# Kernel optimization log

Measured on AMD Instinct MI355X. Metric: run time of the kernel, lower is better.

The kernel has to match this reference:

```python
import jax, jax.numpy as jnp
from jax import lax
import numpy as np

B, T, N, HORIZON = 64, 12, 512, 12
IN_DIM = 1; OUT_DIM = 1; YCOV = 1
RNN = 64; MEM_NUM = 20; MEM_DIM = 64; EMB = 10; CHEB_K = 3
DEC_DIM = RNN + MEM_DIM  # 128


def _xavier(key, shape):
    fan_in, fan_out = shape[0], shape[-1]
    std = float(np.sqrt(2.0 / (fan_in + fan_out)))
    return jax.random.normal(key, shape, dtype=jnp.float32) * std


def _cheb_feats(A, x, batched):
    mm = (lambda a, v: jnp.einsum('bnm,bmc->bnc', a, v)) if batched else (lambda a, v: jnp.einsum('nm,bmc->bnc', a, v))
    gs = [x, mm(A, x)]
    for _ in range(CHEB_K - 2):
        gs.append(2.0 * mm(A, gs[-1]) - gs[-2])
    return jnp.concatenate(gs, axis=-1)


def _agcn(x, A, W, b, batched):
    return _cheb_feats(A, x, batched) @ W + b


def _cell(x, state, A, Wg, bg, Wu, bu, batched):
    # AGCRN GRU cell
    hid = state.shape[-1]
    inp = jnp.concatenate([x, state], axis=-1)
    z_r = jax.nn.sigmoid(_agcn(inp, A, Wg, bg, batched))
    z, r = z_r[..., :hid], z_r[..., hid:]
    cand = jnp.concatenate([x, z * state], axis=-1)
    hc = jnp.tanh(_agcn(cand, A, Wu, bu, batched))
    return r * state + (1.0 - r) * hc


def _encode(x, A, Wg, bg, Wu, bu):
    # x: [B,T,N,C] -> last hidden state [B,N,RNN]
    xt = jnp.swapaxes(x, 0, 1)  # [T,B,N,C]
    init = jnp.zeros((x.shape[0], x.shape[2], RNN), x.dtype)
    def step(state, xt_):
        h = _cell(xt_, state, A, Wg, bg, Wu, bu, batched=False)
        return h, None
    h_t, _ = lax.scan(step, init, xt)
    return h_t


def _query_memory(h_t, Memory, Wq):
    q = h_t @ Wq                                   # [B,N,mem_dim]
    att = jax.nn.softmax(q @ Memory.T, axis=-1)    # [B,N,mem_num]
    value = att @ Memory                           # [B,N,mem_dim]
    _, ind = lax.top_k(att, 2)
    pos = Memory[ind[..., 0]]                      # [B,N,mem_dim]
    return value, pos


def setup_inputs() -> dict:
    key = jax.random.key(0)
    ks = jax.random.split(key, 20)
    x = jax.random.normal(ks[0], (B, T, N, IN_DIM), dtype=jnp.float32)
    x_cov = jax.random.normal(ks[1], (B, T, N, 1), dtype=jnp.float32)
    x_his = jax.random.normal(ks[2], (B, T, N, IN_DIM), dtype=jnp.float32)
    y_cov = jax.random.normal(ks[3], (B, HORIZON, N, YCOV), dtype=jnp.float32)
    a = jax.random.uniform(ks[4], (N, N), dtype=jnp.float32)
    adj = a / jnp.sum(a, axis=-1, keepdims=True)
    enc_in = IN_DIM + RNN
    dec_in = OUT_DIM + YCOV + DEC_DIM
    return {
        'x': x, 'x_cov': x_cov, 'x_his': x_his, 'y_cov': y_cov, 'adj': adj,
        'enc_gate_W': _xavier(ks[5], (CHEB_K * enc_in, 2 * RNN)),
        'enc_gate_b': jnp.zeros((2 * RNN,), jnp.float32),
        'enc_upd_W': _xavier(ks[6], (CHEB_K * enc_in, RNN)),
        'enc_upd_b': jnp.zeros((RNN,), jnp.float32),
        'dec_gate_W': _xavier(ks[7], (CHEB_K * dec_in, 2 * DEC_DIM)),
        'dec_gate_b': jnp.zeros((2 * DEC_DIM,), jnp.float32),
        'dec_upd_W': _xavier(ks[8], (CHEB_K * dec_in, DEC_DIM)),
        'dec_upd_b': jnp.zeros((DEC_DIM,), jnp.float32),
        'Memory': _xavier(ks[9], (MEM_NUM, MEM_DIM)),
        'Wq': _xavier(ks[10], (RNN, MEM_DIM)),
        'hyper_W': _xavier(ks[11], (DEC_DIM, EMB)),
        'hyper_b': jnp.zeros((EMB,), jnp.float32),
        'lat_W': _xavier(ks[12], (MEM_DIM, 1)),
        'lat_b': jnp.zeros((1,), jnp.float32),
        'proj_W': _xavier(ks[13], (DEC_DIM, OUT_DIM)),
        'proj_b': jnp.zeros((OUT_DIM,), jnp.float32),
    }


def reference(x, x_cov, x_his, y_cov, adj,
              enc_gate_W, enc_gate_b, enc_upd_W, enc_upd_b,
              dec_gate_W, dec_gate_b, dec_upd_W, dec_upd_b,
              Memory, Wq, hyper_W, hyper_b, lat_W, lat_b, proj_W, proj_b):
    # --- encoder on x and x_his (shared weights, single static support) ---
    h_t = _encode(x, adj, enc_gate_W, enc_gate_b, enc_upd_W, enc_upd_b)
    h_att, pos = _query_memory(h_t, Memory, Wq)
    h_his_t = _encode(x_his, adj, enc_gate_W, enc_gate_b, enc_upd_W, enc_upd_b)
    _, pos_his = _query_memory(h_his_t, Memory, Wq)
    # schema==1 latent distance head (sigmoid activation)
    latent_dis = jax.nn.sigmoid(((pos - pos_his) @ lat_W + lat_b)[..., 0])  # [B,N]
    # --- adaptive decoder support from hypernetwork ---
    h_aug = jnp.concatenate([h_t, h_att], axis=-1)          # [B,N,DEC_DIM]
    node_emb = h_aug @ hyper_W + hyper_b                    # [B,N,EMB]
    support = jax.nn.softmax(jax.nn.relu(jnp.einsum('bnc,bmc->bnm', node_emb, node_emb)), axis=-1)  # [B,N,N]
    # --- decoder rollout (inference path, no teacher forcing) ---
    go0 = jnp.zeros((x.shape[0], N, OUT_DIM), x.dtype)
    ycov_t = jnp.swapaxes(y_cov, 0, 1)  # [HORIZON,B,N,YCOV]
    def dec_step(carry, yc):
        go, h = carry
        xt = jnp.concatenate([go, yc], axis=-1)
        h = _cell(xt, h, support, dec_gate_W, dec_gate_b, dec_upd_W, dec_upd_b, batched=True)
        go = h @ proj_W + proj_b
        return (go, h), go
    _, outs = lax.scan(dec_step, (go0, h_aug), ycov_t)
    output = jnp.swapaxes(outs, 0, 1)  # [B,HORIZON,N,OUT_DIM]
    return output, latent_dis
```

## Files before the change

### kernel.cpp

```cpp
#include <hip/hip_runtime.h>
#include <hip/hip_bf16.h>


typedef __attribute__((ext_vector_type(8))) short s8v;
typedef __attribute__((ext_vector_type(4))) float f4v;
typedef __attribute__((ext_vector_type(4))) unsigned short u4v;

__device__ __forceinline__ float b2f(unsigned short u){
  union{unsigned int i; float f;} v; v.i = ((unsigned int)u)<<16; return v.f;
}
__device__ __forceinline__ unsigned short f2b(float f){
  union{float f; unsigned int i;} v; v.f = f;
  unsigned int r = v.i + 0x7fff + ((v.i >> 16) & 1);
  return (unsigned short)(r >> 16);
}

__global__ void k_zero16(uint4* p, int n){
  int i = blockIdx.x*256 + threadIdx.x;
  if (i < n) p[i] = make_uint4(0,0,0,0);
}


__global__ void k_reorderF(const float* __restrict__ W, float* __restrict__ Wr,
                           int HC, int NEX, int SEGW, int J){
  int idx = blockIdx.x*256 + threadIdx.x;
  int K = 3*SEGW;
  if (idx >= K*J) return;
  int k = idx / J, j = idx - k*J;
  int seg = k / SEGW, c = k - seg*SEGW;
  int CIN = HC + NEX;
  float v = 0.f;
  if (c < HC)       v = W[(size_t)(seg*CIN + NEX + c)*J + j];
  else if (c < CIN) v = W[(size_t)(seg*CIN + (c-HC))*J + j];
  Wr[(size_t)k*J + j] = v;
}

__global__ __launch_bounds__(256) void k_a2e(const float* __restrict__ A,
                                             float* __restrict__ A2e){
  __shared__ __align__(16) float As[32][132];
  __shared__ __align__(16) float Bs[32][132];
  int t = threadIdx.x;
  int r0 = (blockIdx.x & 3) * 128;
  int c0 = (blockIdx.x >> 2) * 128;
  int tr = t & 15, tc = t >> 4;
  float acc[8][8];
  #pragma unroll
  for (int i=0;i<8;i++)
    #pragma unroll
    for (int j=0;j<8;j++) acc[i][j]=0.f;
  for (int k0=0;k0<512;k0+=32){
    #pragma unroll
    for (int i=0;i<4;i++){
      int s = t + i*256;
      int k = s & 31, rq = s >> 5;
      const float* ap = A + (size_t)(r0 + rq*4)*512 + k0 + k;
      float4 v;
      v.x = ap[0]; v.y = ap[512]; v.z = ap[1024]; v.w = ap[1536];
      *(float4*)&As[k][rq*4] = v;
    }
    #pragma unroll
    for (int i=0;i<4;i++){
      int s = t + i*256;
      int k = s >> 5, cq = s & 31;
      float4 v = *(const float4*)(A + (size_t)(k0+k)*512 + c0 + cq*4);
      *(float4*)&Bs[k][cq*4] = v;
    }
    __syncthreads();
    #pragma unroll 8
    for (int k=0;k<32;k++){
      float a[8], b[8];
      *(float4*)&a[0] = *(const float4*)&As[k][tr*4];
      *(float4*)&a[4] = *(const float4*)&As[k][64+tr*4];
      *(float4*)&b[0] = *(const float4*)&Bs[k][tc*4];
      *(float4*)&b[4] = *(const float4*)&Bs[k][64+tc*4];
      #pragma unroll
      for (int i=0;i<8;i++)
        #pragma unroll
        for (int j=0;j<8;j++) acc[i][j] += a[i]*b[j];
    }
    __syncthreads();
  }
  #pragma unroll
  for (int i=0;i<8;i++){
    int r = r0 + (i<4 ? tr*4+i : 64+tr*4+i-4);
    #pragma unroll
    for (int j=0;j<8;j++){
      int c = c0 + (j<4 ? tc*4+j : 64+tc*4+j-4);
      A2e[(size_t)r*512 + c] = 2.f*acc[i][j] - (r==c ? 1.f : 0.f);
    }
  }
}

template<int MODE>
__global__ __launch_bounds__(256) void k_enc(
    const float* __restrict__ A, const float* __restrict__ A2e,
    const float* __restrict__ hsrc,
    const float* __restrict__ xa, const float* __restrict__ xb,
    int tstep, const float* __restrict__ Wr, const float* __restrict__ bias,
    float* __restrict__ zh, float* __restrict__ rbuf, float* __restrict__ henc)
{
  constexpr int J  = (MODE==0) ? 128 : 64;
  constexpr int TN = (MODE==0) ? 8 : 4;
  __shared__ __align__(16) float R1[8704];
  __shared__ __align__(16) float F0t[2][65][66];
  float (*sA)[68]   = (float(*)[68])(R1);
  float (*sA2)[68]  = (float(*)[68])(R1 + 2176);
  float (*sB0)[68]  = (float(*)[68])(R1 + 4352);
  float (*sB1)[68]  = (float(*)[68])(R1 + 6528);
  float (*G12s)[66] = (float(*)[66])(R1);
  const int t = threadIdx.x;
  const int z = blockIdx.x;
  const int rowblk = blockIdx.z;
  const int n0 = rowblk * 64;
  const int tr = t & 15, tc = t >> 4;
  const int xrow = t & 63, xmat = (t >> 6) & 1, xbb = t >> 7;
  const float* xp0 = xa + ((size_t)z*12 + tstep)*512;
  const float* xp1 = xb + ((size_t)z*12 + tstep)*512;

  float acc[2][2][4][4];
  #pragma unroll
  for (int m=0;m<2;m++)
    #pragma unroll
    for (int b=0;b<2;b++)
      #pragma unroll
      for (int i=0;i<4;i++)
        #pragma unroll
        for (int j=0;j<4;j++) acc[m][b][i][j]=0.f;
  float xacc = 0.f;

  for (int k0=0;k0<512;k0+=32){
    #pragma unroll
    for (int i=0;i<2;i++){
      int s = t + i*256;
      int k = s & 31, rq = s >> 5;
      const float* ap  = A   + (size_t)(n0 + rq*4)*512 + k0 + k;
      const float* a2p = A2e + (size_t)(n0 + rq*4)*512 + k0 + k;
      float4 v, w;
      v.x = ap[0];  v.y = ap[512];  v.z = ap[1024];  v.w = ap[1536];
      w.x = a2p[0]; w.y = a2p[512]; w.z = a2p[1024]; w.w = a2p[1536];
      *(float4*)&sA[k][rq*4]  = v;
      *(float4*)&sA2[k][rq*4] = w;
    }
    #pragma unroll
    for (int i=0;i<2;i++){
      int s = t + i*256;
      int k = s >> 4, cq = s & 15;
      *(float4*)&sB0[k][cq*4] = *(const float4*)(hsrc + (size_t)(z*512 + k0 + k)*64 + cq*4);
      *(float4*)&sB1[k][cq*4] = *(const float4*)(hsrc + (size_t)((z+64)*512 + k0 + k)*64 + cq*4);
    }
    if (t < 32)      sB0[t][64]    = xp0[k0 + t];
    else if (t < 64) sB1[t-32][64] = xp1[k0 + t - 32];
    __syncthreads();
    #pragma unroll 4
    for (int k=0;k<32;k++){
      float a1[4], a2[4], b0[4], b1[4];
      *(float4*)&a1[0] = *(const float4*)&sA[k][tr*4];
      *(float4*)&a2[0] = *(const float4*)&sA2[k][tr*4];
      *(float4*)&b0[0] = *(const float4*)&sB0[k][tc*4];
      *(float4*)&b1[0] = *(const float4*)&sB1[k][tc*4];
      #pragma unroll
      for (int i=0;i<4;i++)
        #pragma unroll
        for (int j=0;j<4;j++){
          acc[0][0][i][j] += a1[i]*b0[j];
          acc[0][1][i][j] += a1[i]*b1[j];
          acc[1][0][i][j] += a2[i]*b0[j];
          acc[1][1][i][j] += a2[i]*b1[j];
        }
      float am = xmat ? sA2[k][xrow] : sA[k][xrow];
      xacc += am * (xbb ? sB1[k][64] : sB0[k][64]);
    }
    if ((k0 >> 6) == rowblk){
      const int off = k0 & 63;
      for (int s=t; s<4160; s+=256){
        int sb = (s >= 2080) ? 1 : 0;
        int ss = s - sb*2080;
        int c = ss >> 5, kk = ss & 31;
        F0t[sb][c][off + kk] = sb ? sB1[kk][c] : sB0[kk][c];
      }
    }
    __syncthreads();
  }

  for (int bbi=0; bbi<2; bbi++){
    #pragma unroll
    for (int m=0;m<2;m++)
      #pragma unroll
      for (int j=0;j<4;j++){
        float4 v;
        v.x = acc[m][bbi][0][j]; v.y = acc[m][bbi][1][j];
        v.z = acc[m][bbi][2][j]; v.w = acc[m][bbi][3][j];
        *(float4*)&G12s[m*65 + tc*4 + j][tr*4] = v;
      }
    if (xbb == bbi) G12s[xmat*65 + 64][xrow] = xacc;
    __syncthreads();

    float acc2[4][TN];
    #pragma unroll
    for (int i=0;i<4;i++)
      #pragma unroll
      for (int jj=0;jj<TN;jj++) acc2[i][jj]=0.f;
    const int j0 = tc*TN;

    #pragma unroll 4
    for (int c=0;c<65;c++){
      float a[4], w[TN];
      *(float4*)&a[0] = *(const float4*)&F0t[bbi][c][tr*4];
      #pragma unroll
      for (int q=0;q<TN;q+=4) *(float4*)&w[q] = *(const float4*)(Wr + (size_t)c*J + j0 + q);
      #pragma unroll
      for (int i=0;i<4;i++)
        #pragma unroll
        for (int jj=0;jj<TN;jj++) acc2[i][jj] += a[i]*w[jj];
    }
    #pragma unroll 4
    for (int c=0;c<65;c++){
      float a[4], w[TN];
      *(float4*)&a[0] = *(const float4*)&G12s[c][tr*4];
      #pragma unroll
      for (int q=0;q<TN;q+=4) *(float4*)&w[q] = *(const float4*)(Wr + (size_t)(68+c)*J + j0 + q);
      #pragma unroll
      for (int i=0;i<4;i++)
        #pragma unroll
        for (int jj=0;jj<TN;jj++) acc2[i][jj] += a[i]*w[jj];
    }
    #pragma unroll 4
    for (int c=0;c<65;c++){
      float a[4], w[TN];
      *(float4*)&a[0] = *(const float4*)&G12s[65+c][tr*4];
      #pragma unroll
      for (int q=0;q<TN;q+=4) *(float4*)&w[q] = *(const float4*)(Wr + (size_t)(136+c)*J + j0 + q);
      #pragma unroll
      for (int i=0;i<4;i++)
        #pragma unroll
        for (int jj=0;jj<TN;jj++) acc2[i][jj] += a[i]*w[jj];
    }

    float bj[TN];
    #pragma unroll
    for (int jj=0;jj<TN;jj++) bj[jj] = bias[j0+jj];
    const int gbase = (z + bbi*64)*512 + n0;
    #pragma unroll
    for (int i=0;i<4;i++){
      const int lr = tr*4 + i;
      const int row = gbase + lr;
      if (MODE == 0){
        float s[8];
        #pragma unroll
        for (int jj=0;jj<TN;jj++) s[jj] = 1.f/(1.f + __expf(-(acc2[i][jj] + bj[jj])));
        if (j0 < 64){
          float4 o0, o1;
          o0.x = s[0]*F0t[bbi][j0+0][lr]; o0.y = s[1]*F0t[bbi][j0+1][lr];
          o0.z = s[2]*F0t[bbi][j0+2][lr]; o0.w = s[3]*F0t[bbi][j0+3][lr];
          o1.x = s[4]*F0t[bbi][j0+4][lr]; o1.y = s[5]*F0t[bbi][j0+5][lr];
          o1.z = s[6]*F0t[bbi][j0+6][lr]; o1.w = s[7]*F0t[bbi][j0+7][lr];
          *(float4*)(zh + (size_t)row*64 + j0)     = o0;
          *(float4*)(zh + (size_t)row*64 + j0 + 4) = o1;
        } else {
          float4 o0, o1;
          o0.x=s[0]; o0.y=s[1]; o0.z=s[2]; o0.w=s[3];
          o1.x=s[4]; o1.y=s[5]; o1.z=s[6]; o1.w=s[7];
          *(float4*)(rbuf + (size_t)row*64 + j0 - 64) = o0;
          *(float4*)(rbuf + (size_t)row*64 + j0 - 60) = o1;
        }
      } else {
        float4 h4 = *(const float4*)(henc + (size_t)row*64 + j0);
        float4 r4 = *(const float4*)(rbuf + (size_t)row*64 + j0);
        float hv[4] = {h4.x,h4.y,h4.z,h4.w};
        float rv[4] = {r4.x,r4.y,r4.z,r4.w};
        float ov[4];
        #pragma unroll
        for (int jj=0;jj<4;jj++){
          float hc = 1.f - 2.f/(__expf(2.f*(acc2[i][jj] + bj[jj])) + 1.f);
          ov[jj] = rv[jj]*hv[jj] + (1.f - rv[jj])*hc;
        }
        float4 o; o.x=ov[0]; o.y=ov[1]; o.z=ov[2]; o.w=ov[3];
        *(float4*)(henc + (size_t)row*64 + j0) = o;
      }
    }
    __syncthreads();
  }
}


__global__ void k_reorderB(const float* __restrict__ W, unsigned short* __restrict__ Wr,
                           int HC, int NEX, int C, int KP, int J){
  int idx = blockIdx.x*256 + threadIdx.x;
  if (idx >= J*KP) return;
  int j = idx / KP, kp = idx - j*KP;
  float v = 0.f;
  if (kp < 3*C){
    int seg = kp / C, c = kp - seg*C;
    int CIN = HC + NEX;
    if (c < HC)       v = W[(size_t)(seg*CIN + NEX + c)*J + j];
    else if (c < CIN) v = W[(size_t)(seg*CIN + (c-HC))*J + j];
  }
  Wr[(size_t)j*KP + kp] = f2b(v);
}

template<int C16, bool BETA>
__global__ __launch_bounds__(256) void k_mmB(
    const unsigned short* __restrict__ M, long long mstride,
    unsigned short* fC, int C3, int xseg, int oseg,
    unsigned short* fR, int KP, float alpha)
{
  constexpr int C = C16*16;
  constexpr int BIT = (C*4 + 255)/256;
  __shared__ unsigned short Bs[C*40];
  const int t = threadIdx.x;
  const int w = t >> 6, L = t & 63, lm = L & 15, q = L >> 4;
  const int bb = blockIdx.z;
  const int n0 = blockIdx.x * 128;
  const unsigned short* Mb = M + (size_t)bb * mstride;
  unsigned short* fCb = fC + (size_t)bb * C3 * 512;
  const unsigned short* Xb = fCb + (size_t)xseg * C * 512;
  const unsigned short* Yb = fCb;
  unsigned short* Ob = fCb + (size_t)oseg * C * 512;
  const int rw = n0 + w*32;

  f4v acc[2][C16];
  #pragma unroll
  for (int i=0;i<2;i++)
    #pragma unroll
    for (int j=0;j<C16;j++)
      #pragma unroll
      for (int r=0;r<4;r++) acc[i][j][r] = 0.f;

  s8v breg[BIT];
  const size_t ar0 = (size_t)(rw + lm)*512 + q*8;
  const size_t ar1 = (size_t)(rw + 16 + lm)*512 + q*8;

  #pragma unroll
  for (int i=0;i<BIT;i++){
    int s = t + i*256;
    if (s < C*4) breg[i] = *(const s8v*)(Xb + (size_t)(s>>2)*512 + (s&3)*8);
  }
  s8v a0 = *(const s8v*)(Mb + ar0);
  s8v a1 = *(const s8v*)(Mb + ar1);

  for (int ks=0; ks<16; ks++){
    #pragma unroll
    for (int i=0;i<BIT;i++){
      int s = t + i*256;
      if (s < C*4) *(s8v*)&Bs[(s>>2)*40 + (s&3)*8] = breg[i];
    }
    __syncthreads();
    const int kn = (ks < 15) ? (ks+1)*32 : 0;
    #pragma unroll
    for (int i=0;i<BIT;i++){
      int s = t + i*256;
      if (s < C*4) breg[i] = *(const s8v*)(Xb + (size_t)(s>>2)*512 + kn + (s&3)*8);
    }
    s8v a0n = *(const s8v*)(Mb + ar0 + kn);
    s8v a1n = *(const s8v*)(Mb + ar1 + kn);
    #pragma unroll
    for (int ct=0; ct<C16; ct++){
      s8v b = *(const s8v*)&Bs[(ct*16+lm)*40 + q*8];
      acc[0][ct] = __builtin_amdgcn_mfma_f32_16x16x32_bf16(a0, b, acc[0][ct], 0,0,0);
      acc[1][ct] = __builtin_amdgcn_mfma_f32_16x16x32_bf16(a1, b, acc[1][ct], 0,0,0);
    }
    __syncthreads();
    a0 = a0n; a1 = a1n;
  }
  #pragma unroll
  for (int rt=0; rt<2; rt++){
    const int m0 = rw + rt*16 + q*4;
    #pragma unroll
    for (int ct=0; ct<C16; ct++){
      const int c = ct*16 + lm;
      u4v o;
      if (BETA){
        u4v y = *(const u4v*)(Yb + (size_t)c*512 + m0);
        #pragma unroll
        for (int r=0;r<4;r++) o[r] = f2b(alpha*acc[rt][ct][r] - b2f(y[r]));
      } else {
        #pragma unroll
        for (int r=0;r<4;r++) o[r] = f2b(acc[rt][ct][r]);
      }
      *(u4v*)(Ob + (size_t)c*512 + m0) = o;
      const size_t rbase = (size_t)(bb*512 + m0)*KP + oseg*C + c;
      #pragma unroll
      for (int r=0;r<4;r++) fR[rbase + (size_t)r*KP] = o[r];
    }
  }
}

template<int KSTEPS, int JT16, int MODE, int HC>
__global__ __launch_bounds__(256) void k_gwB(
    unsigned short* fR, int KP,
    const unsigned short* __restrict__ Wr, const float* __restrict__ bias,
    unsigned short* fC, int C3,
    float* hC, float* rbuf)
{
  constexpr int JT = JT16*16;
  constexpr int BIT = JT*4/256;
  __shared__ unsigned short Bs[JT*40];
  const int t = threadIdx.x;
  const int w = t >> 6, L = t & 63, lm = L & 15, q = L >> 4;
  const int row0 = blockIdx.x * 128;
  const int j0 = blockIdx.y * JT;
  const int rw = row0 + w*32;

  f4v acc[2][JT16];
  #pragma unroll
  for (int i=0;i<2;i++)
    #pragma unroll
    for (int j=0;j<JT16;j++)
      #pragma unroll
      for (int r=0;r<4;r++) acc[i][j][r] = 0.f;

  s8v breg[BIT];
  const unsigned short* Wb = Wr + (size_t)j0*KP;
  const size_t ar0 = (size_t)(rw + lm)*KP + q*8;
  const size_t ar1 = (size_t)(rw + 16 + lm)*KP + q*8;

  #pragma unroll
  for (int i=0;i<BIT;i++){
    int s = t + i*256;
    breg[i] = *(const s8v*)(Wb + (size_t)(s>>2)*KP + (s&3)*8);
  }
  s8v a0 = *(const s8v*)(fR + ar0);
  s8v a1 = *(const s8v*)(fR + ar1);

  for (int ks=0; ks<KSTEPS; ks++){
    #pragma unroll
    for (int i=0;i<BIT;i++){
      int s = t + i*256;
      *(s8v*)&Bs[(s>>2)*40 + (s&3)*8] = breg[i];
    }
    __syncthreads();
    const int kn = (ks < KSTEPS-1) ? (ks+1)*32 : 0;
    #pragma unroll
    for (int i=0;i<BIT;i++){
      int s = t + i*256;
      breg[i] = *(const s8v*)(Wb + (size_t)(s>>2)*KP + kn + (s&3)*8);
    }
    s8v a0n = *(const s8v*)(fR + ar0 + kn);
    s8v a1n = *(const s8v*)(fR + ar1 + kn);
    #pragma unroll
    for (int ct=0; ct<JT16; ct++){
      s8v b = *(const s8v*)&Bs[(ct*16+lm)*40 + q*8];
      acc[0][ct] = __builtin_amdgcn_mfma_f32_16x16x32_bf16(a0, b, acc[0][ct], 0,0,0);
      acc[1][ct] = __builtin_amdgcn_mfma_f32_16x16x32_bf16(a1, b, acc[1][ct], 0,0,0);
    }
    __syncthreads();
    a0 = a0n; a1 = a1n;
  }
  #pragma unroll
  for (int rt=0; rt<2; rt++){
    const int m0 = rw + rt*16 + q*4;
    const int bb = m0 >> 9, n = m0 & 511;
    #pragma unroll
    for (int ct=0; ct<JT16; ct++){
      const int j = j0 + ct*16 + lm;
      const float bj = bias[j];
      if (MODE == 0){
        if (j < HC){
          f4v h4 = *(const f4v*)(hC + ((size_t)bb*HC + j)*512 + n);
          u4v o;
          #pragma unroll
          for (int r=0;r<4;r++){
            float s = 1.f/(1.f + __expf(-(acc[rt][ct][r] + bj)));
            float zh = s * h4[r];
            o[r] = f2b(zh);
            fR[(size_t)(m0+r)*KP + j] = o[r];
          }
          *(u4v*)(fC + ((size_t)bb*C3 + j)*512 + n) = o;
        } else {
          f4v rv;
          #pragma unroll
          for (int r=0;r<4;r++) rv[r] = 1.f/(1.f + __expf(-(acc[rt][ct][r] + bj)));
          *(f4v*)(rbuf + ((size_t)bb*HC + (j-HC))*512 + n) = rv;
        }
      } else {
        f4v h4 = *(const f4v*)(hC + ((size_t)bb*HC + j)*512 + n);
        f4v r4 = *(const f4v*)(rbuf + ((size_t)bb*HC + j)*512 + n);
        u4v o; f4v hn;
        #pragma unroll
        for (int r=0;r<4;r++){
          float e = __expf(2.f*(acc[rt][ct][r] + bj));
          float hc_ = 1.f - 2.f/(e + 1.f);
          hn[r] = r4[r]*h4[r] + (1.f - r4[r])*hc_;
          o[r] = f2b(hn[r]);
          fR[(size_t)(m0+r)*KP + j] = o[r];
        }
        *(f4v*)(hC + ((size_t)bb*HC + j)*512 + n) = hn;
        *(u4v*)(fC + ((size_t)bb*C3 + j)*512 + n) = o;
      }
    }
  }
}


__global__ void k_extras_dec(const float* __restrict__ yc,
    unsigned short* fR, unsigned short* fC, int tstep){
  int rr = blockIdx.x*256 + threadIdx.x;
  int bb = rr >> 9, n = rr & 511;
  unsigned short u = f2b(yc[((size_t)bb*12 + tstep)*512 + n]);
  fR[(size_t)rr*448 + 129] = u;
  fC[((size_t)bb*432 + 129)*512 + n] = u;
}
__global__ void k_fix_go(unsigned short* fR, unsigned short* fC){
  int rr = blockIdx.x*256 + threadIdx.x;
  int bb = rr >> 9, n = rr & 511;
  fR[(size_t)rr*448 + 128] = 0;
  fC[((size_t)bb*432 + 128)*512 + n] = 0;
}

__global__ __launch_bounds__(256) void k_query(const float* __restrict__ hR,
      const float* __restrict__ Wq, const float* __restrict__ Mem,
      float* __restrict__ hCd, unsigned short* fR, unsigned short* fC,
      int* __restrict__ it, int* __restrict__ ih){
  int sub = threadIdx.x >> 6, lane = threadIdx.x & 63;
  int row = blockIdx.x*4 + sub;
  __shared__ float sh[4][64], sq[4][64], ss[4][20];
  float hv = hR[(size_t)row*64 + lane];
  sh[sub][lane] = hv;
  __syncthreads();
  float qv = 0.f;
  for (int c=0;c<64;c++) qv += sh[sub][c]*Wq[c*64 + lane];
  sq[sub][lane] = qv;
  __syncthreads();
  if (lane < 20){
    float s = 0.f;
    for (int j=0;j<64;j++) s += sq[sub][j]*Mem[lane*64 + j];
    ss[sub][lane] = s;
  }
  __syncthreads();
  float mx = -1e30f; int am = 0;
  for (int m=0;m<20;m++){ float s = ss[sub][m]; if (s > mx){ mx = s; am = m; } }
  float sum = 0.f;
  for (int m=0;m<20;m++) sum += __expf(ss[sub][m]-mx);
  float inv = 1.f/sum;
  float v = 0.f;
  for (int m=0;m<20;m++) v += __expf(ss[sub][m]-mx)*inv*Mem[m*64 + lane];
  int bb = row >> 9, n = row & 511;
  if (bb < 64){
    hCd[((size_t)bb*128 + lane)*512 + n] = hv;
    hCd[((size_t)bb*128 + 64 + lane)*512 + n] = v;
    fR[(size_t)row*448 + lane] = f2b(hv);
    fR[(size_t)row*448 + 64 + lane] = f2b(v);
    fC[((size_t)bb*432 + lane)*512 + n] = f2b(hv);
    fC[((size_t)bb*432 + 64 + lane)*512 + n] = f2b(v);
    if (lane==0) it[row] = am;
  } else {
    if (lane==0) ih[row - 32768] = am;
  }
}

__global__ void k_latent(const int* __restrict__ it, const int* __restrict__ ih,
                         const float* __restrict__ Mem,
                         const float* __restrict__ lW, const float* __restrict__ lb,
                         float* __restrict__ outl){
  int row = blockIdx.x*256 + threadIdx.x;
  int i1 = it[row], i2 = ih[row];
  float a = lb[0];
  for (int c=0;c<64;c++) a += (Mem[i1*64+c]-Mem[i2*64+c])*lW[c];
  outl[row] = 1.f/(1.f + __expf(-a));
}

__global__ __launch_bounds__(256) void k_emb(const float* __restrict__ hCd,
    const float* __restrict__ hW, const float* __restrict__ hb, float* __restrict__ emb){
  __shared__ float sW[1280];
  int t = threadIdx.x;
  for (int s=t; s<1280; s+=256) sW[s] = hW[s];
  __syncthreads();
  int rr = blockIdx.x*256 + t;
  int bb = rr >> 9, n = rr & 511;
  float a[10];
  #pragma unroll
  for (int e=0;e<10;e++) a[e] = hb[e];
  for (int c=0;c<128;c++){
    float v = hCd[((size_t)bb*128 + c)*512 + n];
    #pragma unroll
    for (int e=0;e<10;e++) a[e] += v*sW[c*10+e];
  }
  #pragma unroll
  for (int e=0;e<10;e++) emb[(size_t)rr*10 + e] = a[e];
}

__global__ __launch_bounds__(256) void k_support(const float* __restrict__ emb,
                                                 unsigned short* __restrict__ sup){
  int b = blockIdx.x >> 9;
  int n = blockIdx.x & 511;
  int t = threadIdx.x;
  __shared__ float se[5120];
  __shared__ float red[8];
  for (int s = t; s < 5120; s += 256) se[s] = emb[(size_t)b*5120 + s];
  __syncthreads();
  float en[10];
  #pragma unroll
  for (int i=0;i<10;i++) en[i] = se[n*10+i];
  float s0=0.f, s1=0.f;
  #pragma unroll
  for (int i=0;i<10;i++){ s0 += en[i]*se[t*10+i]; s1 += en[i]*se[(t+256)*10+i]; }
  s0 = fmaxf(s0, 0.f); s1 = fmaxf(s1, 0.f);
  float mx = fmaxf(s0, s1);
  for (int o=32;o>0;o>>=1) mx = fmaxf(mx, __shfl_down(mx, o));
  if ((t&63)==0) red[t>>6] = mx;
  __syncthreads();
  mx = fmaxf(fmaxf(red[0],red[1]), fmaxf(red[2],red[3]));
  float e0 = __expf(s0-mx), e1 = __expf(s1-mx);
  float sm = e0 + e1;
  for (int o=32;o>0;o>>=1) sm += __shfl_down(sm, o);
  if ((t&63)==0) red[4+(t>>6)] = sm;
  __syncthreads();
  sm = red[4]+red[5]+red[6]+red[7];
  float inv = 1.f/sm;
  size_t base = ((size_t)b*512 + n)*512;
  sup[base + t]       = f2b(e0*inv);
  sup[base + t + 256] = f2b(e1*inv);
}

__global__ __launch_bounds__(256) void k_proj(const float* __restrict__ hCd,
    const float* __restrict__ pW, const float* __restrict__ pb,
    unsigned short* fR, unsigned short* fC, float* __restrict__ out, int tstep){
  __shared__ float sW[128];
  int t = threadIdx.x;
  if (t < 128) sW[t] = pW[t];
  __syncthreads();
  int rr = blockIdx.x*256 + t;
  int bb = rr >> 9, n = rr & 511;
  float a = pb[0];
  for (int c=0;c<128;c++) a += hCd[((size_t)bb*128 + c)*512 + n]*sW[c];
  out[((size_t)bb*12 + tstep)*512 + n] = a;
  unsigned short u = f2b(a);
  fR[(size_t)rr*448 + 128] = u;
  fC[((size_t)bb*432 + 128)*512 + n] = u;
}

extern "C" void kernel_launch(void* const* d_in, const int* in_sizes, int n_in,
                              void* d_out, int out_size, void* d_ws, size_t ws_size,
                              hipStream_t stream) {
  const float* x     = (const float*)d_in[0];
  const float* x_his = (const float*)d_in[2];
  const float* y_cov = (const float*)d_in[3];
  const float* adj   = (const float*)d_in[4];
  const float* egW   = (const float*)d_in[5];
  const float* egb   = (const float*)d_in[6];
  const float* euW   = (const float*)d_in[7];
  const float* eub   = (const float*)d_in[8];
  const float* dgW   = (const float*)d_in[9];
  const float* dgb   = (const float*)d_in[10];
  const float* duW   = (const float*)d_in[11];
  const float* dub   = (const float*)d_in[12];
  const float* Mem   = (const float*)d_in[13];
  const float* Wq    = (const float*)d_in[14];
  const float* hW    = (const float*)d_in[15];
  const float* hb    = (const float*)d_in[16];
  const float* lW    = (const float*)d_in[17];
  const float* lb    = (const float*)d_in[18];
  const float* pW    = (const float*)d_in[19];
  const float* pb    = (const float*)d_in[20];
  float* out  = (float*)d_out;
  float* outl = out + 393216;

  char* base = (char*)d_ws;
  size_t off = 0;
  auto alloc = [&](size_t bytes)->char*{
    char* p = base + off; off = (off + bytes + 255) & ~(size_t)255; return p;
  };
  float* scratch = (float*)alloc(53477376);
  unsigned short* sup = (unsigned short*)scratch;
  float* emb = scratch + 8650752;
  int*   it  = (int*)(scratch + 9961472);
  int*   ih  = it + 32768;
  float* henc = (float*)alloc(16777216);
  float* zhF  = (float*)alloc(16777216);
  float* hCd  = zhF;
  float* rbF  = (float*)alloc(16777216);
  unsigned short* fR = (unsigned short*)alloc(29360128);
  unsigned short* fC = (unsigned short*)alloc(28311552);
  float* a2e = (float*)alloc(1048576);
  float* wr_egF = (float*)alloc(104448);
  float* wr_euF = (float*)alloc(52224);
  unsigned short* wr_dg = (unsigned short*)alloc(229376);
  unsigned short* wr_du = (unsigned short*)alloc(114688);
  if (ws_size < off) return;

  k_zero16<<<4096,256,0,stream>>>((uint4*)henc, 1048576);
  k_zero16<<<7168,256,0,stream>>>((uint4*)fR, 1835008);
  k_zero16<<<6912,256,0,stream>>>((uint4*)fC, 1769472);
  k_a2e<<<16,256,0,stream>>>(adj, a2e);
  k_reorderF<<<102,256,0,stream>>>(egW, wr_egF, 64,1,68,128);
  k_reorderF<<< 51,256,0,stream>>>(euW, wr_euF, 64,1,68,64);
  k_reorderB<<<448,256,0,stream>>>(dgW, wr_dg, 128,2,144,448,256);
  k_reorderB<<<224,256,0,stream>>>(duW, wr_du, 128,2,144,448,128);

  for (int t = 0; t < 12; t++){
    k_enc<0><<<dim3(64,1,8),256,0,stream>>>(adj, a2e, henc, x, x_his, t,
                                            wr_egF, egb, zhF, rbF, nullptr);
    k_enc<1><<<dim3(64,1,8),256,0,stream>>>(adj, a2e, zhF, x, x_his, t,
                                            wr_euF, eub, nullptr, rbF, henc);
  }

  k_query<<<16384,256,0,stream>>>(henc, Wq, Mem, hCd, fR, fC, it, ih);
  k_latent<<<128,256,0,stream>>>(it, ih, Mem, lW, lb, outl);
  k_emb<<<128,256,0,stream>>>(hCd, hW, hb, emb);
  k_support<<<32768,256,0,stream>>>(emb, sup);
  k_fix_go<<<128,256,0,stream>>>(fR, fC);

  for (int t = 0; t < 12; t++){
    k_extras_dec<<<128,256,0,stream>>>(y_cov, fR, fC, t);
    k_mmB<9,false><<<dim3(4,1,64),256,0,stream>>>(sup, 262144, fC, 432, 0, 1, fR, 448, 1.f);
    k_mmB<9,true ><<<dim3(4,1,64),256,0,stream>>>(sup, 262144, fC, 432, 1, 2, fR, 448, 2.f);
    k_gwB<14,16,0,128><<<dim3(256,1),256,0,stream>>>(fR, 448, wr_dg, dgb, fC, 432, hCd, rbF);
    k_mmB<9,false><<<dim3(4,1,64),256,0,stream>>>(sup, 262144, fC, 432, 0, 1, fR, 448, 1.f);
    k_mmB<9,true ><<<dim3(4,1,64),256,0,stream>>>(sup, 262144, fC, 432, 1, 2, fR, 448, 2.f);
    k_gwB<14,8,1,128><<<dim3(256,1),256,0,stream>>>(fR, 448, wr_du, dub, fC, 432, hCd, rbF);
    k_proj<<<128,256,0,stream>>>(hCd, pW, pb, fR, fC, out, t);
  }
}
```

Baseline: 6.503 ms.

## Precompute second Chebyshev support and fuse decoder graph matmuls into one kernel

Adds a one-time batched MFMA kernel that builds the second Chebyshev support 2S²−I in bf16, so each decoder cell computes S·X and S2·X independently in a single fused kernel instead of two dependent launches. This removes the serial dependency and one launch per cell, and halves the per-block row tile to raise parallelism. The encoder kernel also halves its k-tile and reuses one shared buffer for the two Chebyshev feature halves, which cuts LDS use but adds a barrier and doubles loop iterations. The trade-off is extra bf16 rounding in the precomputed S2 and an additional 32MB workspace buffer.

```diff
diff --git a/kernel.cpp b/kernel.cpp
--- a/kernel.cpp
+++ b/kernel.cpp
@@ -101,13 +101,13 @@
 {
   constexpr int J  = (MODE==0) ? 128 : 64;
   constexpr int TN = (MODE==0) ? 8 : 4;
-  __shared__ __align__(16) float R1[8704];
+  __shared__ __align__(16) float R1[4352];
   __shared__ __align__(16) float F0t[2][65][66];
   float (*sA)[68]   = (float(*)[68])(R1);
-  float (*sA2)[68]  = (float(*)[68])(R1 + 2176);
-  float (*sB0)[68]  = (float(*)[68])(R1 + 4352);
-  float (*sB1)[68]  = (float(*)[68])(R1 + 6528);
-  float (*G12s)[66] = (float(*)[66])(R1);
+  float (*sA2)[68]  = (float(*)[68])(R1 + 1088);
+  float (*sB0)[68]  = (float(*)[68])(R1 + 2176);
+  float (*sB1)[68]  = (float(*)[68])(R1 + 3264);
+  float (*G12h)[66] = (float(*)[66])(R1);
   const int t = threadIdx.x;
   const int z = blockIdx.x;
   const int rowblk = blockIdx.z;
@@ -128,11 +128,9 @@
         for (int j=0;j<4;j++) acc[m][b][i][j]=0.f;
   float xacc = 0.f;
 
-  for (int k0=0;k0<512;k0+=32){
-    #pragma unroll
-    for (int i=0;i<2;i++){
-      int s = t + i*256;
-      int k = s & 31, rq = s >> 5;
+  for (int k0=0;k0<512;k0+=16){
+    {
+      int k = t & 15, rq = t >> 4;
       const float* ap  = A   + (size_t)(n0 + rq*4)*512 + k0 + k;
       const float* a2p = A2e + (size_t)(n0 + rq*4)*512 + k0 + k;
       float4 v, w;
@@ -141,18 +139,16 @@
       *(float4*)&sA[k][rq*4]  = v;
       *(float4*)&sA2[k][rq*4] = w;
     }
-    #pragma unroll
-    for (int i=0;i<2;i++){
-      int s = t + i*256;
-      int k = s >> 4, cq = s & 15;
+    {
+      int k = t >> 4, cq = t & 15;
       *(float4*)&sB0[k][cq*4] = *(const float4*)(hsrc + (size_t)(z*512 + k0 + k)*64 + cq*4);
       *(float4*)&sB1[k][cq*4] = *(const float4*)(hsrc + (size_t)((z+64)*512 + k0 + k)*64 + cq*4);
     }
-    if (t < 32)      sB0[t][64]    = xp0[k0 + t];
-    else if (t < 64) sB1[t-32][64] = xp1[k0 + t - 32];
+    if (t < 16)      sB0[t][64]    = xp0[k0 + t];
+    else if (t < 32) sB1[t-16][64] = xp1[k0 + t - 16];
     __syncthreads();
     #pragma unroll 4
-    for (int k=0;k<32;k++){
+    for (int k=0;k<16;k++){
       float a1[4], a2[4], b0[4], b1[4];
       *(float4*)&a1[0] = *(const float4*)&sA[k][tr*4];
       *(float4*)&a2[0] = *(const float4*)&sA2[k][tr*4];
@@ -172,10 +168,10 @@
     }
     if ((k0 >> 6) == rowblk){
       const int off = k0 & 63;
-      for (int s=t; s<4160; s+=256){
-        int sb = (s >= 2080) ? 1 : 0;
-        int ss = s - sb*2080;
-        int c = ss >> 5, kk = ss & 31;
+      for (int s=t; s<2080; s+=256){
+        int sb = (s >= 1040) ? 1 : 0;
+        int ss = s - sb*1040;
+        int c = ss >> 4, kk = ss & 15;
         F0t[sb][c][off + kk] = sb ? sB1[kk][c] : sB0[kk][c];
       }
     }
@@ -184,15 +180,13 @@
 
   for (int bbi=0; bbi<2; bbi++){
     #pragma unroll
-    for (int m=0;m<2;m++)
-      #pragma unroll
-      for (int j=0;j<4;j++){
-        float4 v;
-        v.x = acc[m][bbi][0][j]; v.y = acc[m][bbi][1][j];
-        v.z = acc[m][bbi][2][j]; v.w = acc[m][bbi][3][j];
-        *(float4*)&G12s[m*65 + tc*4 + j][tr*4] = v;
-      }
-    if (xbb == bbi) G12s[xmat*65 + 64][xrow] = xacc;
+    for (int j=0;j<4;j++){
+      float4 v;
+      v.x = acc[0][bbi][0][j]; v.y = acc[0][bbi][1][j];
+      v.z = acc[0][bbi][2][j]; v.w = acc[0][bbi][3][j];
+      *(float4*)&G12h[tc*4 + j][tr*4] = v;
+    }
+    if (xbb == bbi && xmat == 0) G12h[64][xrow] = xacc;
     __syncthreads();
 
     float acc2[4][TN];
@@ -216,7 +210,7 @@
     #pragma unroll 4
     for (int c=0;c<65;c++){
       float a[4], w[TN];
-      *(float4*)&a[0] = *(const float4*)&G12s[c][tr*4];
+      *(float4*)&a[0] = *(const float4*)&G12h[c][tr*4];
       #pragma unroll
       for (int q=0;q<TN;q+=4) *(float4*)&w[q] = *(const float4*)(Wr + (size_t)(68+c)*J + j0 + q);
       #pragma unroll
@@ -224,10 +218,20 @@
         #pragma unroll
         for (int jj=0;jj<TN;jj++) acc2[i][jj] += a[i]*w[jj];
     }
+    __syncthreads();
+    #pragma unroll
+    for (int j=0;j<4;j++){
+      float4 v;
+      v.x = acc[1][bbi][0][j]; v.y = acc[1][bbi][1][j];
+      v.z = acc[1][bbi][2][j]; v.w = acc[1][bbi][3][j];
+      *(float4*)&G12h[tc*4 + j][tr*4] = v;
+    }
+    if (xbb == bbi && xmat == 1) G12h[64][xrow] = xacc;
+    __syncthreads();
     #pragma unroll 4
     for (int c=0;c<65;c++){
       float a[4], w[TN];
-      *(float4*)&a[0] = *(const float4*)&G12s[65+c][tr*4];
+      *(float4*)&a[0] = *(const float4*)&G12h[c][tr*4];
       #pragma unroll
       for (int q=0;q<TN;q+=4) *(float4*)&w[q] = *(const float4*)(Wr + (size_t)(136+c)*J + j0 + q);
       #pragma unroll
@@ -298,89 +302,132 @@
   Wr[(size_t)j*KP + kp] = f2b(v);
 }
 
-template<int C16, bool BETA>
-__global__ __launch_bounds__(256) void k_mmB(
-    const unsigned short* __restrict__ M, long long mstride,
-    unsigned short* fC, int C3, int xseg, int oseg,
-    unsigned short* fR, int KP, float alpha)
+__global__ __launch_bounds__(256) void k_sup2(const unsigned short* __restrict__ S,
+                                              unsigned short* __restrict__ S2){
+  __shared__ unsigned short Bs[128*40];
+  const int t = threadIdx.x;
+  const int w = t >> 6, L = t & 63, lm = L & 15, q = L >> 4;
+  const int bb = blockIdx.z;
+  const int n0 = blockIdx.x * 128;
+  const int m0 = blockIdx.y * 128;
+  const unsigned short* Sb = S + (size_t)bb * 262144;
+  unsigned short* S2b = S2 + (size_t)bb * 262144;
+  f4v acc[2][8];
+  #pragma unroll
+  for (int i=0;i<2;i++)
+    #pragma unroll
+    for (int j=0;j<8;j++)
+      #pragma unroll
+      for (int r=0;r<4;r++) acc[i][j][r] = 0.f;
+  for (int k0=0;k0<512;k0+=32){
+    #pragma unroll
+    for (int i=0;i<2;i++){
+      int s = t + i*256;
+      int kk = s >> 4, mg = s & 15;
+      s8v v = *(const s8v*)(Sb + (size_t)(k0+kk)*512 + m0 + mg*8);
+      #pragma unroll
+      for (int e=0;e<8;e++) Bs[(mg*8+e)*40 + kk] = ((unsigned short*)&v)[e];
+    }
+    __syncthreads();
+    s8v a0 = *(const s8v*)(Sb + (size_t)(n0 + w*32 + lm)*512 + k0 + q*8);
+    s8v a1 = *(const s8v*)(Sb + (size_t)(n0 + w*32 + 16 + lm)*512 + k0 + q*8);
+    #pragma unroll
+    for (int ct=0;ct<8;ct++){
+      s8v b = *(const s8v*)&Bs[(ct*16+lm)*40 + q*8];
+      acc[0][ct] = __builtin_amdgcn_mfma_f32_16x16x32_bf16(a0, b, acc[0][ct], 0,0,0);
+      acc[1][ct] = __builtin_amdgcn_mfma_f32_16x16x32_bf16(a1, b, acc[1][ct], 0,0,0);
+    }
+    __syncthreads();
+  }
+  #pragma unroll
+  for (int rt=0;rt<2;rt++){
+    const int row = n0 + w*32 + rt*16 + q*4;
+    #pragma unroll
+    for (int ct=0;ct<8;ct++){
+      const int col = m0 + ct*16 + lm;
+      #pragma unroll
+      for (int r=0;r<4;r++){
+        float v = 2.f*acc[rt][ct][r] - ((row+r)==col ? 1.f : 0.f);
+        S2b[(size_t)(row+r)*512 + col] = f2b(v);
+      }
+    }
+  }
+}
+
+__global__ __launch_bounds__(256) void k_mmB2(
+    const unsigned short* __restrict__ M1, const unsigned short* __restrict__ M2,
+    unsigned short* fC, unsigned short* fR)
 {
-  constexpr int C = C16*16;
-  constexpr int BIT = (C*4 + 255)/256;
+  constexpr int C = 144;
   __shared__ unsigned short Bs[C*40];
   const int t = threadIdx.x;
   const int w = t >> 6, L = t & 63, lm = L & 15, q = L >> 4;
   const int bb = blockIdx.z;
-  const int n0 = blockIdx.x * 128;
-  const unsigned short* Mb = M + (size_t)bb * mstride;
-  unsigned short* fCb = fC + (size_t)bb * C3 * 512;
-  const unsigned short* Xb = fCb + (size_t)xseg * C * 512;
-  const unsigned short* Yb = fCb;
-  unsigned short* Ob = fCb + (size_t)oseg * C * 512;
-  const int rw = n0 + w*32;
-
-  f4v acc[2][C16];
+  const int n0 = blockIdx.x * 64;
+  const unsigned short* M1b = M1 + (size_t)bb * 262144;
+  const unsigned short* M2b = M2 + (size_t)bb * 262144;
+  unsigned short* fCb = fC + (size_t)bb * 432 * 512;
+  const unsigned short* Xb = fCb;
+  unsigned short* O1 = fCb + (size_t)C * 512;
+  unsigned short* O2 = fCb + (size_t)2 * C * 512;
+  const int rw = n0 + w*16;
+
+  f4v acc[2][9];
   #pragma unroll
   for (int i=0;i<2;i++)
     #pragma unroll
-    for (int j=0;j<C16;j++)
+    for (int j=0;j<9;j++)
       #pragma unroll
       for (int r=0;r<4;r++) acc[i][j][r] = 0.f;
 
-  s8v breg[BIT];
-  const size_t ar0 = (size_t)(rw + lm)*512 + q*8;
-  const size_t ar1 = (size_t)(rw + 16 + lm)*512 + q*8;
-
-  #pragma unroll
-  for (int i=0;i<BIT;i++){
+  s8v breg[3];
+  const size_t ar = (size_t)(rw + lm)*512 + q*8;
+  #pragma unroll
+  for (int i=0;i<3;i++){
     int s = t + i*256;
     if (s < C*4) breg[i] = *(const s8v*)(Xb + (size_t)(s>>2)*512 + (s&3)*8);
   }
-  s8v a0 = *(const s8v*)(Mb + ar0);
-  s8v a1 = *(const s8v*)(Mb + ar1);
+  s8v a1 = *(const s8v*)(M1b + ar);
+  s8v a2 = *(const s8v*)(M2b + ar);
 
   for (int ks=0; ks<16; ks++){
     #pragma unroll
-    for (int i=0;i<BIT;i++){
+    for (int i=0;i<3;i++){
       int s = t + i*256;
       if (s < C*4) *(s8v*)&Bs[(s>>2)*40 + (s&3)*8] = breg[i];
     }
     __syncthreads();
     const int kn = (ks < 15) ? (ks+1)*32 : 0;
     #pragma unroll
-    for (int i=0;i<BIT;i++){
+    for (int i=0;i<3;i++){
       int s = t + i*256;
       if (s < C*4) breg[i] = *(const s8v*)(Xb + (size_t)(s>>2)*512 + kn + (s&3)*8);
     }
-    s8v a0n = *(const s8v*)(Mb + ar0 + kn);
-    s8v a1n = *(const s8v*)(Mb + ar1 + kn);
-    #pragma unroll
-    for (int ct=0; ct<C16; ct++){
+    s8v a1n = *(const s8v*)(M1b + ar + kn);
+    s8v a2n = *(const s8v*)(M2b + ar + kn);
+    #pragma unroll
+    for (int ct=0; ct<9; ct++){
       s8v b = *(const s8v*)&Bs[(ct*16+lm)*40 + q*8];
-      acc[0][ct] = __builtin_amdgcn_mfma_f32_16x16x32_bf16(a0, b, acc[0][ct], 0,0,0);
-      acc[1][ct] = __builtin_amdgcn_mfma_f32_16x16x32_bf16(a1, b, acc[1][ct], 0,0,0);
-    }
-    __syncthreads();
-    a0 = a0n; a1 = a1n;
-  }
-  #pragma unroll
-  for (int rt=0; rt<2; rt++){
-    const int m0 = rw + rt*16 + q*4;
-    #pragma unroll
-    for (int ct=0; ct<C16; ct++){
-      const int c = ct*16 + lm;
-      u4v o;
-      if (BETA){
-        u4v y = *(const u4v*)(Yb + (size_t)c*512 + m0);
-        #pragma unroll
-        for (int r=0;r<4;r++) o[r] = f2b(alpha*acc[rt][ct][r] - b2f(y[r]));
-      } else {
-        #pragma unroll
-        for (int r=0;r<4;r++) o[r] = f2b(acc[rt][ct][r]);
-      }
-      *(u4v*)(Ob + (size_t)c*512 + m0) = o;
-      const size_t rbase = (size_t)(bb*512 + m0)*KP + oseg*C + c;
-      #pragma unroll
-      for (int r=0;r<4;r++) fR[rbase + (size_t)r*KP] = o[r];
+      acc[0][ct] = __builtin_amdgcn_mfma_f32_16x16x32_bf16(a1, b, acc[0][ct], 0,0,0);
+      acc[1][ct] = __builtin_amdgcn_mfma_f32_16x16x32_bf16(a2, b, acc[1][ct], 0,0,0);
+    }
+    __syncthreads();
+    a1 = a1n; a2 = a2n;
+  }
+  const int m0 = rw + q*4;
+  #pragma unroll
+  for (int ct=0; ct<9; ct++){
+    const int c = ct*16 + lm;
+    u4v o1, o2;
+    #pragma unroll
+    for (int r=0;r<4;r++){ o1[r] = f2b(acc[0][ct][r]); o2[r] = f2b(acc[1][ct][r]); }
+    *(u4v*)(O1 + (size_t)c*512 + m0) = o1;
+    *(u4v*)(O2 + (size_t)c*512 + m0) = o2;
+    const size_t rb = (size_t)(bb*512 + m0)*448;
+    #pragma unroll
+    for (int r=0;r<4;r++){
+      fR[rb + (size_t)r*448 + 144 + c] = o1[r];
+      fR[rb + (size_t)r*448 + 288 + c] = o2[r];
     }
   }
 }
@@ -660,11 +707,11 @@
   auto alloc = [&](size_t bytes)->char*{
     char* p = base + off; off = (off + bytes + 255) & ~(size_t)255; return p;
   };
-  float* scratch = (float*)alloc(53477376);
-  unsigned short* sup = (unsigned short*)scratch;
-  float* emb = scratch + 8650752;
-  int*   it  = (int*)(scratch + 9961472);
-  int*   ih  = it + 32768;
+  unsigned short* sup  = (unsigned short*)alloc(33554432);
+  unsigned short* sup2 = (unsigned short*)alloc(33554432);
+  float* emb  = (float*)alloc(1310720);
+  int*   it   = (int*)alloc(131072);
+  int*   ih   = (int*)alloc(131072);
   float* henc = (float*)alloc(16777216);
   float* zhF  = (float*)alloc(16777216);
   float* hCd  = zhF;
@@ -698,15 +745,14 @@
   k_latent<<<128,256,0,stream>>>(it, ih, Mem, lW, lb, outl);
   k_emb<<<128,256,0,stream>>>(hCd, hW, hb, emb);
   k_support<<<32768,256,0,stream>>>(emb, sup);
+  k_sup2<<<dim3(4,4,64),256,0,stream>>>(sup, sup2);
   k_fix_go<<<128,256,0,stream>>>(fR, fC);
 
   for (int t = 0; t < 12; t++){
     k_extras_dec<<<128,256,0,stream>>>(y_cov, fR, fC, t);
-    k_mmB<9,false><<<dim3(4,1,64),256,0,stream>>>(sup, 262144, fC, 432, 0, 1, fR, 448, 1.f);
-    k_mmB<9,true ><<<dim3(4,1,64),256,0,stream>>>(sup, 262144, fC, 432, 1, 2, fR, 448, 2.f);
+    k_mmB2<<<dim3(8,1,64),256,0,stream>>>(sup, sup2, fC, fR);
     k_gwB<14,16,0,128><<<dim3(256,1),256,0,stream>>>(fR, 448, wr_dg, dgb, fC, 432, hCd, rbF);
-    k_mmB<9,false><<<dim3(4,1,64),256,0,stream>>>(sup, 262144, fC, 432, 0, 1, fR, 448, 1.f);
-    k_mmB<9,true ><<<dim3(4,1,64),256,0,stream>>>(sup, 262144, fC, 432, 1, 2, fR, 448, 2.f);
+    k_mmB2<<<dim3(8,1,64),256,0,stream>>>(sup, sup2, fC, fR);
     k_gwB<14,8,1,128><<<dim3(256,1),256,0,stream>>>(fR, 448, wr_du, dub, fC, 432, hCd, rbF);
     k_proj<<<128,256,0,stream>>>(hCd, pW, pb, fR, fC, out, t);
   }
```

Result: faster. 6.101 ms (-6.2%).
